# Optimization experiments

Measured on AMD Instinct MI355X. Metric: run time of the kernel, lower is better.

The kernel has to match this reference:

```python
import jax, jax.numpy as jnp
import numpy as np

D_MODEL = 1024
NUM_HEADS = 16
D_K = D_MODEL // NUM_HEADS


def setup_inputs() -> dict:
    key = jax.random.key(0)
    ks = jax.random.split(key, 9)
    B, S = 4, 2048
    s = 1.0 / np.sqrt(D_MODEL)
    inp = {
        "x": jax.random.normal(ks[0], (B, S, D_MODEL), dtype=jnp.float32),
        "wq": jax.random.uniform(ks[1], (D_MODEL, D_MODEL), jnp.float32, -s, s),
        "bq": jax.random.uniform(ks[2], (D_MODEL,), jnp.float32, -s, s),
        "wk": jax.random.uniform(ks[3], (D_MODEL, D_MODEL), jnp.float32, -s, s),
        "bk": jax.random.uniform(ks[4], (D_MODEL,), jnp.float32, -s, s),
        "wv": jax.random.uniform(ks[5], (D_MODEL, D_MODEL), jnp.float32, -s, s),
        "bv": jax.random.uniform(ks[6], (D_MODEL,), jnp.float32, -s, s),
        "wo": jax.random.uniform(ks[7], (D_MODEL, D_MODEL), jnp.float32, -s, s),
        "bo": jax.random.uniform(ks[8], (D_MODEL,), jnp.float32, -s, s),
    }
    return inp


def reference(x, wq, bq, wk, bk, wv, bv, wo, bo):
    B, S, _ = x.shape
    H, Dk = NUM_HEADS, D_K
    # QKV projections; weights stored as (in, out) so y = x @ w + b
    q = (x @ wq + bq).reshape(B, S, H, Dk).transpose(0, 2, 1, 3)  # (B,H,S,Dk)
    k = (x @ wk + bk).reshape(B, S, H, Dk).transpose(0, 2, 1, 3)
    v = (x @ wv + bv).reshape(B, S, H, Dk).transpose(0, 2, 1, 3)
    scores = jnp.einsum("bhqd,bhkd->bhqk", q, k) / jnp.sqrt(jnp.float32(Dk))
    causal = jnp.tril(jnp.ones((S, S), dtype=bool))  # True = keep
    scores = jnp.where(causal, scores, jnp.float32(-jnp.inf))
    attn = jax.nn.softmax(scores, axis=-1)  # dropout=0 (eval)
    out = jnp.einsum("bhqk,bhkd->bhqd", attn, v)
    out = out.transpose(0, 2, 1, 3).reshape(B, S, H * Dk)
    return out @ wo + bo
```

## Files before the change

kernel.cpp:

```cpp
#include <hip/hip_runtime.h>
#include <hip/hip_bf16.h>


#define D_MODEL 1024
#define NHEADS  16
#define DK      64
#define BATCH   4
#define SEQ     2048
#define MROWS   (BATCH*SEQ)

typedef short bvec8 __attribute__((ext_vector_type(8)));
typedef float fvec4  __attribute__((ext_vector_type(4)));
typedef float fvec16 __attribute__((ext_vector_type(16)));

__device__ __forceinline__ unsigned short f2bf(float f) {
    unsigned int x = __float_as_uint(f);
    x += 0x7fffu + ((x >> 16) & 1u);
    return (unsigned short)(x >> 16);
}
__device__ __forceinline__ float bf2f(unsigned short u) {
    return __uint_as_float(((unsigned int)u) << 16);
}

__device__ __forceinline__ unsigned pack_bf16x2(float a, float b) {
#if __has_builtin(__builtin_amdgcn_cvt_pk_bf16_f32)
    typedef __bf16 bf16x2_t __attribute__((ext_vector_type(2)));
    union { bf16x2_t v; unsigned u; } cv;
    cv.v = __builtin_amdgcn_cvt_pk_bf16_f32(a, b);
    return cv.u;
#else
    return (unsigned)f2bf(a) | ((unsigned)f2bf(b) << 16);
#endif
}

__device__ __forceinline__ float fast_exp2(float x) {
#if __has_builtin(__builtin_amdgcn_exp2f)
    return __builtin_amdgcn_exp2f(x);
#else
    return exp2f(x);
#endif
}


__global__ void f32_to_bf16_k(const float* __restrict__ in,
                              unsigned short* __restrict__ out, int n4) {
    int i = blockIdx.x * 256 + threadIdx.x;
    if (i < n4) {
        float4 v = ((const float4*)in)[i];
        ushort4 o;
        o.x = f2bf(v.x); o.y = f2bf(v.y); o.z = f2bf(v.z); o.w = f2bf(v.w);
        ((ushort4*)out)[i] = o;
    }
}

__global__ void transpose_all_k(const float* __restrict__ wq, const float* __restrict__ wk,
                                const float* __restrict__ wv, const float* __restrict__ wo,
                                unsigned short* __restrict__ wqkvt,
                                unsigned short* __restrict__ wot) {
    __shared__ float tile[32][33];
    const int z = blockIdx.z;
    const float* W = (z == 0) ? wq : (z == 1) ? wk : (z == 2) ? wv : wo;
    unsigned short* Wt = (z == 3) ? wot : wqkvt + (size_t)z * D_MODEL * D_MODEL;
    int n0 = blockIdx.x * 32, k0 = blockIdx.y * 32;
    int tx = threadIdx.x & 31;
    int ty = (threadIdx.x >> 5) * 4;
#pragma unroll
    for (int i = 0; i < 4; ++i)
        tile[ty + i][tx] = W[(k0 + ty + i) * D_MODEL + n0 + tx];
    __syncthreads();
#pragma unroll
    for (int i = 0; i < 4; ++i)
        Wt[(n0 + ty + i) * D_MODEL + k0 + tx] = f2bf(tile[tx][ty + i]);
}

__global__ void build_cbias_k(const float* __restrict__ bq, const float* __restrict__ bk,
                              const float* __restrict__ bv, float* __restrict__ cb) {
    int i = blockIdx.x * 256 + threadIdx.x;
    float v = (i < 1024) ? bq[i] : (i < 2048) ? bk[i - 1024] : bv[i - 2048];
    cb[i] = v;
}

__global__ __launch_bounds__(256, 2)
void gemm_glds(const unsigned short* __restrict__ A,
               const unsigned short* __restrict__ Bt,
               const float* __restrict__ bias,
               unsigned short* __restrict__ oq,
               unsigned short* __restrict__ ok,
               unsigned short* __restrict__ ov,
               float* __restrict__ of,
               float qscale, int mode) {
    __shared__ __align__(16) unsigned short As[2][128 * 64];
    __shared__ __align__(16) unsigned short Bs[2][128 * 64];

    const int tid  = threadIdx.x;
    const int lane = tid & 63;
    const int w    = tid >> 6;
    const int wr   = w >> 1, wc = w & 1;
    const int quad = lane >> 4, l16 = lane & 15;
    const int rowBlock = blockIdx.y * 128;
    const int colBlock = blockIdx.x * 128;

    const int lrow   = lane >> 3;
    const int gchunk = (lane & 7) ^ lrow;

    fvec4 acc[4][4] = {};

    {
#pragma unroll
        for (int n = 0; n < 4; ++n) {
            const int g = w * 4 + n;
            __builtin_amdgcn_global_load_lds(
                (const __attribute__((address_space(1))) void*)
                    &A[(size_t)(rowBlock + g * 8 + lrow) * D_MODEL + gchunk * 8],
                (__attribute__((address_space(3))) void*)&As[0][g * 512], 16, 0, 0);
            __builtin_amdgcn_global_load_lds(
                (const __attribute__((address_space(1))) void*)
                    &Bt[(size_t)(colBlock + g * 8 + lrow) * D_MODEL + gchunk * 8],
                (__attribute__((address_space(3))) void*)&Bs[0][g * 512], 16, 0, 0);
        }
    }

    for (int i = 0; i < 16; ++i) {
        __syncthreads();
        const int buf = i & 1;
        if (i < 15) {
            const int k1 = (i + 1) * 64;
#pragma unroll
            for (int n = 0; n < 4; ++n) {
                const int g = w * 4 + n;
                __builtin_amdgcn_global_load_lds(
                    (const __attribute__((address_space(1))) void*)
                        &A[(size_t)(rowBlock + g * 8 + lrow) * D_MODEL + k1 + gchunk * 8],
                    (__attribute__((address_space(3))) void*)&As[buf ^ 1][g * 512], 16, 0, 0);
                __builtin_amdgcn_global_load_lds(
                    (const __attribute__((address_space(1))) void*)
                        &Bt[(size_t)(colBlock + g * 8 + lrow) * D_MODEL + k1 + gchunk * 8],
                    (__attribute__((address_space(3))) void*)&Bs[buf ^ 1][g * 512], 16, 0, 0);
            }
        }
#pragma unroll
        for (int kc = 0; kc < 2; ++kc) {
            bvec8 af[4], bfr[4];
#pragma unroll
            for (int ii = 0; ii < 4; ++ii) {
                int r = wr * 64 + ii * 16 + l16;
                af[ii] = *(const bvec8*)&As[buf][r * 64 + (((kc * 4 + quad) ^ (l16 & 7)) * 8)];
            }
#pragma unroll
            for (int j = 0; j < 4; ++j) {
                int r = wc * 64 + j * 16 + l16;
                bfr[j] = *(const bvec8*)&Bs[buf][r * 64 + (((kc * 4 + quad) ^ (l16 & 7)) * 8)];
            }
#pragma unroll
            for (int ii = 0; ii < 4; ++ii)
#pragma unroll
                for (int j = 0; j < 4; ++j)
                    acc[ii][j] = __builtin_amdgcn_mfma_f32_16x16x32_bf16(
                        af[ii], bfr[j], acc[ii][j], 0, 0, 0);
        }
    }

    if (mode == 0) {
#pragma unroll
        for (int i = 0; i < 4; ++i) {
#pragma unroll
            for (int j = 0; j < 4; ++j) {
                int ncol = colBlock + wc * 64 + j * 16 + l16;
                int which = ncol >> 10;
                int nn = ncol & 1023;
                int h = nn >> 6, d = nn & 63;
                float bv = bias[ncol];
#pragma unroll
                for (int r = 0; r < 4; ++r) {
                    int mrow = rowBlock + wr * 64 + i * 16 + quad * 4 + r;
                    int b = mrow >> 11, s = mrow & (SEQ - 1);
                    float v = acc[i][j][r] + bv;
                    if (which == 0)
                        oq[(((b * NHEADS + h) * SEQ + s) * DK) + d] = f2bf(v * qscale);
                    else if (which == 1)
                        ok[(((b * NHEADS + h) * SEQ + s) * DK) + d] = f2bf(v);
                    else
                        ov[(((b * NHEADS + h) * DK + d) * SEQ) + s] = f2bf(v);
                }
            }
        }
    } else {
#pragma unroll
        for (int i = 0; i < 4; ++i) {
#pragma unroll
            for (int j = 0; j < 4; ++j) {
                int ncol = colBlock + wc * 64 + j * 16 + l16;
                float bv = bias[ncol];
#pragma unroll
                for (int r = 0; r < 4; ++r) {
                    int mrow = rowBlock + wr * 64 + i * 16 + quad * 4 + r;
                    of[(size_t)mrow * D_MODEL + ncol] = acc[i][j][r] + bv;
                }
            }
        }
    }
}

__global__ __launch_bounds__(256, 4)
void attn_mfmaA(const unsigned short* __restrict__ Q,
                const unsigned short* __restrict__ K,
                const unsigned short* __restrict__ Vt,
                unsigned short* __restrict__ O,
                unsigned short* __restrict__ Opart,
                float* __restrict__ Lpart) {
    __shared__ __align__(16) unsigned short Ksm[2][64 * 64];
    __shared__ __align__(16) unsigned short Vsm[2][64 * 64];
    __shared__ float Lsh[4][32];

    const int tid  = threadIdx.x;
    const int lane = tid & 63;
    const int wq   = tid >> 6;
    const int hf   = lane >> 5;
    const int l32  = lane & 31;
    const int hh = blockIdx.y, b = blockIdx.z;
    const int hb = b * NHEADS + hh;

    static const int qt_tbl[24] = {15,15,7,14,14,6,13,13,12,12,5,11,
                                   11,10,10,4,9,9,8,8,3,2,1,0};
    static const int md_tbl[24] = {0,1,2,0,1,2,0,1,0,1,2,0,
                                   1,0,1,2,0,1,0,1,2,2,2,2};
    const int bx = blockIdx.x;
    const int qt = qt_tbl[bx];
    const int md = md_tbl[bx];
    const bool part = (md < 2);
    const int kt0 = (md == 1) ? qt + 1 : 0;
    const int kt1 = (md == 0) ? qt + 1 : 2 * qt + 2;
    const int slot = part ? ((qt - 8) * 2 + md) : 0;

    const size_t bhq = ((size_t)hb) * SEQ * DK;
    const unsigned short* Qb = Q + bhq;
    const unsigned short* Kb = K + bhq;
    const unsigned short* Vb = Vt + bhq;

    const int q0 = qt * 128 + wq * 32;

    bvec8 qf[4];
#pragma unroll
    for (int kc = 0; kc < 4; ++kc)
        qf[kc] = *(const bvec8*)&Qb[(q0 + l32) * DK + kc * 16 + hf * 8];

    const int sr = tid >> 2;
    const int sc = tid & 3;
    const int sp0 = ((sc) ^ (sr & 7)) * 8;
    const int sp1 = ((sc + 4) ^ (sr & 7)) * 8;

    const int ktact = 2 * qt + (wq >> 1);
    const int mofs  = (wq & 1) << 5;

    bvec8 kr0, kr1, vr0, vr1;
    {
        const unsigned short* kg = Kb + (kt0 * 64 + sr) * DK;
        kr0 = *(const bvec8*)(kg + sc * 8);
        kr1 = *(const bvec8*)(kg + (sc + 4) * 8);
        const unsigned short* vg = Vb + sr * SEQ + kt0 * 64;
        vr0 = *(const bvec8*)(vg + sc * 8);
        vr1 = *(const bvec8*)(vg + (sc + 4) * 8);
        *(bvec8*)&Ksm[0][sr * 64 + sp0] = kr0;
        *(bvec8*)&Ksm[0][sr * 64 + sp1] = kr1;
        *(bvec8*)&Vsm[0][sr * 64 + sp0] = vr0;
        *(bvec8*)&Vsm[0][sr * 64 + sp1] = vr1;
    }

    fvec16 acc0 = {};
    fvec16 acc1 = {};
    float lp = 0.f;

    for (int kt = kt0; kt < kt1; ++kt) {
        __syncthreads();
        const int buf = (kt - kt0) & 1;
        if (kt + 1 < kt1) {
            const unsigned short* kg = Kb + ((kt + 1) * 64 + sr) * DK;
            kr0 = *(const bvec8*)(kg + sc * 8);
            kr1 = *(const bvec8*)(kg + (sc + 4) * 8);
            const unsigned short* vg = Vb + sr * SEQ + (kt + 1) * 64;
            vr0 = *(const bvec8*)(vg + sc * 8);
            vr1 = *(const bvec8*)(vg + (sc + 4) * 8);
        }
        if (kt <= ktact) {
            const unsigned short* Kbuf = &Ksm[buf][0];
            const unsigned short* Vbuf = &Vsm[buf][0];

            fvec16 s0 = {}, s1 = {};
            __builtin_amdgcn_s_setprio(1);
#pragma unroll
            for (int kc = 0; kc < 4; ++kc) {
                const int ch = (((kc * 2 + hf) ^ (l32 & 7)) * 8);
                bvec8 a0 = *(const bvec8*)&Kbuf[l32 * 64 + ch];
                bvec8 a1 = *(const bvec8*)&Kbuf[(32 + l32) * 64 + ch];
                s0 = __builtin_amdgcn_mfma_f32_32x32x16_bf16(a0, qf[kc], s0, 0, 0, 0);
                s1 = __builtin_amdgcn_mfma_f32_32x32x16_bf16(a1, qf[kc], s1, 0, 0, 0);
            }
            __builtin_amdgcn_s_setprio(0);

            if (kt == ktact) {
#pragma unroll
                for (int r = 0; r < 16; ++r) {
                    const int key0 = (r & 3) + 8 * (r >> 2) + 4 * hf - mofs;
                    if (key0 > l32)      s0[r] = -__builtin_inff();
                    if (key0 + 32 > l32) s1[r] = -__builtin_inff();
                }
            }

            unsigned pk[16];
#pragma unroll
            for (int m = 0; m < 8; ++m) {
                float p0 = fast_exp2(s0[2 * m]);
                float p1 = fast_exp2(s0[2 * m + 1]);
                float p2 = fast_exp2(s1[2 * m]);
                float p3 = fast_exp2(s1[2 * m + 1]);
                lp += (p0 + p1) + (p2 + p3);
                pk[m]     = pack_bf16x2(p0, p1);
                pk[8 + m] = pack_bf16x2(p2, p3);
            }

            __builtin_amdgcn_s_setprio(1);
#pragma unroll
            for (int kc16 = 0; kc16 < 4; ++kc16) {
                const int b0 = (kc16 >> 1) * 8 + (kc16 & 1) * 4;
                unsigned sw0 = __shfl_xor(pk[b0 + 0], 32);
                unsigned sw1 = __shfl_xor(pk[b0 + 1], 32);
                unsigned sw2 = __shfl_xor(pk[b0 + 2], 32);
                unsigned sw3 = __shfl_xor(pk[b0 + 3], 32);
                union { unsigned u[4]; bvec8 v; } afu;
                afu.u[0] = hf ? sw2 : pk[b0 + 0];
                afu.u[1] = hf ? sw3 : pk[b0 + 1];
                afu.u[2] = hf ? pk[b0 + 2] : sw0;
                afu.u[3] = hf ? pk[b0 + 3] : sw1;
                const int ch = (((kc16 * 2 + hf) ^ (l32 & 7)) * 8);
                bvec8 bv0 = *(const bvec8*)&Vbuf[l32 * 64 + ch];
                bvec8 bv1 = *(const bvec8*)&Vbuf[(32 + l32) * 64 + ch];
                acc0 = __builtin_amdgcn_mfma_f32_32x32x16_bf16(afu.v, bv0, acc0, 0, 0, 0);
                acc1 = __builtin_amdgcn_mfma_f32_32x32x16_bf16(afu.v, bv1, acc1, 0, 0, 0);
            }
            __builtin_amdgcn_s_setprio(0);
        }
        if (kt + 1 < kt1) {
            const int nb = ((kt - kt0) & 1) ^ 1;
            *(bvec8*)&Ksm[nb][sr * 64 + sp0] = kr0;
            *(bvec8*)&Ksm[nb][sr * 64 + sp1] = kr1;
            *(bvec8*)&Vsm[nb][sr * 64 + sp0] = vr0;
            *(bvec8*)&Vsm[nb][sr * 64 + sp1] = vr1;
        }
    }

    const float l = lp + __shfl_xor(lp, 32);

    if (part) {
        if (lane < 32)
            Lpart[((size_t)slot * 64 + hb) * 128 + wq * 32 + l32] = l;
        unsigned short* Od = Opart + (((size_t)slot * 64 + hb) * 128 + wq * 32) * 64;
#pragma unroll
        for (int g = 0; g < 4; ++g)
#pragma unroll
            for (int rr = 0; rr < 4; ++rr) {
                const int reg = g * 4 + rr;
                const int qrl = g * 8 + 4 * hf + rr;
                Od[(size_t)qrl * 64 + l32]      = f2bf(acc0[reg]);
                Od[(size_t)qrl * 64 + 32 + l32] = f2bf(acc1[reg]);
            }
    } else {
        if (lane < 32) Lsh[wq][l32] = l;
#pragma unroll
        for (int g = 0; g < 4; ++g) {
            float4 lv = *(const float4*)&Lsh[wq][g * 8 + 4 * hf];
#pragma unroll
            for (int rr = 0; rr < 4; ++rr) {
                const int reg = g * 4 + rr;
                const int qrow = q0 + g * 8 + 4 * hf + rr;
                const float inv = 1.f / ((const float*)&lv)[rr];
                unsigned short* dst = O + (size_t)(b * SEQ + qrow) * D_MODEL + hh * DK + l32;
                dst[0]  = f2bf(acc0[reg] * inv);
                dst[32] = f2bf(acc1[reg] * inv);
            }
        }
    }
}

__global__ void attn_combine_k(const unsigned short* __restrict__ Opart,
                               const float* __restrict__ Lpart,
                               unsigned short* __restrict__ O) {
    const int qt = 8 + blockIdx.x;
    const int h = blockIdx.y, b = blockIdx.z;
    const int hb = b * NHEADS + h;
    const int s0 = (qt - 8) * 2;
    const unsigned short* A  = Opart + ((size_t)(s0)*64 + hb) * 128 * 64;
    const unsigned short* Bp = Opart + ((size_t)(s0 + 1) * 64 + hb) * 128 * 64;
    const float* LA = Lpart + ((size_t)(s0)*64 + hb) * 128;
    const float* LB = Lpart + ((size_t)(s0 + 1) * 64 + hb) * 128;
    for (int e = threadIdx.x; e < 128 * 64; e += 256) {
        const int qr = e >> 6, d = e & 63;
        const float inv = 1.f / (LA[qr] + LB[qr]);
        const float v = (bf2f(A[e]) + bf2f(Bp[e])) * inv;
        O[(size_t)(b * SEQ + qt * 128 + qr) * D_MODEL + h * DK + d] = f2bf(v);
    }
}


extern "C" void kernel_launch(void* const* d_in, const int* in_sizes, int n_in,
                              void* d_out, int out_size, void* d_ws, size_t ws_size,
                              hipStream_t stream) {
    const float* x  = (const float*)d_in[0];
    const float* wq = (const float*)d_in[1];
    const float* bq = (const float*)d_in[2];
    const float* wk = (const float*)d_in[3];
    const float* bk = (const float*)d_in[4];
    const float* wv = (const float*)d_in[5];
    const float* bv = (const float*)d_in[6];
    const float* wo = (const float*)d_in[7];
    const float* bo = (const float*)d_in[8];
    float* out = (float*)d_out;

    char* ws = (char*)d_ws;
    const size_t MB = 1u << 20;
    unsigned short* xb    = (unsigned short*)(ws);
    unsigned short* wqkvt = (unsigned short*)(ws + 16 * MB);
    unsigned short* wot   = (unsigned short*)(ws + 22 * MB);
    unsigned short* qb    = (unsigned short*)(ws + 24 * MB);
    unsigned short* kb    = (unsigned short*)(ws + 40 * MB);
    unsigned short* vtb   = (unsigned short*)(ws + 56 * MB);
    unsigned short* ab    = (unsigned short*)(ws + 72 * MB);
    float* cbias = (float*)(ws + 72 * MB);
    unsigned short* Opart = (unsigned short*)(ws);
    float* Lpart = (float*)(ws + 16 * MB);

    f32_to_bf16_k<<<(MROWS * D_MODEL / 4 + 255) / 256, 256, 0, stream>>>(
        x, xb, MROWS * D_MODEL / 4);
    transpose_all_k<<<dim3(32, 32, 4), 256, 0, stream>>>(wq, wk, wv, wo, wqkvt, wot);
    build_cbias_k<<<12, 256, 0, stream>>>(bq, bk, bv, cbias);

    const float QSCALE = 0.125f * 1.44269504088896340736f;

    gemm_glds<<<dim3(3072 / 128, MROWS / 128), 256, 0, stream>>>(
        xb, wqkvt, cbias, qb, kb, vtb, nullptr, QSCALE, 0);

    attn_mfmaA<<<dim3(24, NHEADS, BATCH), 256, 0, stream>>>(
        qb, kb, vtb, ab, Opart, Lpart);
    attn_combine_k<<<dim3(8, NHEADS, BATCH), 256, 0, stream>>>(Opart, Lpart, ab);

    gemm_glds<<<dim3(D_MODEL / 128, MROWS / 128), 256, 0, stream>>>(
        ab, wot, bo, nullptr, nullptr, nullptr, out, 1.0f, 1);
}
```

Baseline: 295.1 us.

## Add 256x256-tile QKV GEMM with 4-stage direct-to-LDS pipeline

Measured after the change: 320.6 us. 8.6% more time.

```diff
diff --git a/kernel.cpp b/kernel.cpp
--- a/kernel.cpp
+++ b/kernel.cpp
@@ -80,15 +80,123 @@
     cb[i] = v;
 }
 
+__global__ __launch_bounds__(512, 2)
+void gemm_qkv_q8(const unsigned short* __restrict__ A,
+                 const unsigned short* __restrict__ Bt,
+                 const float* __restrict__ bias,
+                 unsigned short* __restrict__ oq,
+                 unsigned short* __restrict__ ok,
+                 unsigned short* __restrict__ ov,
+                 float qscale) {
+    __shared__ __align__(16) unsigned short Abuf[4][256 * 32];
+    __shared__ __align__(16) unsigned short Bbuf[4][256 * 32];
+
+    const int tid  = threadIdx.x;
+    const int lane = tid & 63;
+    const int w    = tid >> 6;
+    const int wm   = w >> 2;
+    const int wn   = w & 3;
+    const int quad = lane >> 4, l16 = lane & 15;
+    const int rowBlock = blockIdx.y * 256;
+    const int colBlock = blockIdx.x * 256;
+
+    const int srow = tid >> 2;
+    const int skc  = (tid & 3) ^ ((srow >> 1) & 3);
+    const size_t aoff0 = (size_t)(rowBlock + srow) * D_MODEL + skc * 8;
+    const size_t boff0 = (size_t)(colBlock + srow) * D_MODEL + skc * 8;
+    const size_t roff1 = (size_t)128 * D_MODEL;
+
+#define Q8_STAGE(u) do {                                                      \
+    const int _b = (u) & 3; const int _k = (u) * 32;                          \
+    __builtin_amdgcn_global_load_lds(                                         \
+        (const __attribute__((address_space(1))) void*)(A + aoff0 + _k),      \
+        (__attribute__((address_space(3))) void*)&Abuf[_b][tid * 8], 16, 0, 0); \
+    __builtin_amdgcn_global_load_lds(                                         \
+        (const __attribute__((address_space(1))) void*)(A + aoff0 + roff1 + _k), \
+        (__attribute__((address_space(3))) void*)&Abuf[_b][(tid + 512) * 8], 16, 0, 0); \
+    __builtin_amdgcn_global_load_lds(                                         \
+        (const __attribute__((address_space(1))) void*)(Bt + boff0 + _k),     \
+        (__attribute__((address_space(3))) void*)&Bbuf[_b][tid * 8], 16, 0, 0); \
+    __builtin_amdgcn_global_load_lds(                                         \
+        (const __attribute__((address_space(1))) void*)(Bt + boff0 + roff1 + _k), \
+        (__attribute__((address_space(3))) void*)&Bbuf[_b][(tid + 512) * 8], 16, 0, 0); \
+} while (0)
+
+    fvec4 acc[8][4] = {};
+    const int sw = quad ^ ((l16 >> 1) & 3);
+
+    Q8_STAGE(0); Q8_STAGE(1); Q8_STAGE(2);
+
+#define Q8_COMPUTE(PH) do {                                                   \
+    const unsigned short* Au = &Abuf[(PH) & 3][0];                            \
+    const unsigned short* Bu = &Bbuf[(PH) & 3][0];                            \
+    bvec8 af[8], bfr[4];                                                      \
+    _Pragma("unroll")                                                         \
+    for (int mf = 0; mf < 8; ++mf) {                                          \
+        const int row = wm * 128 + mf * 16 + l16;                             \
+        af[mf] = *(const bvec8*)&Au[(row * 4 + sw) * 8];                      \
+    }                                                                         \
+    _Pragma("unroll")                                                         \
+    for (int nf = 0; nf < 4; ++nf) {                                          \
+        const int nrow = wn * 64 + nf * 16 + l16;                             \
+        bfr[nf] = *(const bvec8*)&Bu[(nrow * 4 + sw) * 8];                    \
+    }                                                                         \
+    __builtin_amdgcn_s_setprio(1);                                            \
+    _Pragma("unroll")                                                         \
+    for (int mf = 0; mf < 8; ++mf)                                            \
+        _Pragma("unroll")                                                     \
+        for (int nf = 0; nf < 4; ++nf)                                        \
+            acc[mf][nf] = __builtin_amdgcn_mfma_f32_16x16x32_bf16(            \
+                af[mf], bfr[nf], acc[mf][nf], 0, 0, 0);                       \
+    __builtin_amdgcn_s_setprio(0);                                            \
+} while (0)
+
+    for (int ph = 0; ph < 30; ++ph) {
+        asm volatile("s_waitcnt vmcnt(8)" ::: "memory");
+        __builtin_amdgcn_s_barrier();
+        if (ph < 29) Q8_STAGE(ph + 3);
+        Q8_COMPUTE(ph);
+    }
+    asm volatile("s_waitcnt vmcnt(4)" ::: "memory");
+    __builtin_amdgcn_s_barrier();
+    Q8_COMPUTE(30);
+    asm volatile("s_waitcnt vmcnt(0)" ::: "memory");
+    __builtin_amdgcn_s_barrier();
+    Q8_COMPUTE(31);
+
+#undef Q8_STAGE
+#undef Q8_COMPUTE
+
+#pragma unroll
+    for (int mf = 0; mf < 8; ++mf) {
+#pragma unroll
+        for (int nf = 0; nf < 4; ++nf) {
+            const int ncol = colBlock + wn * 64 + nf * 16 + l16;
+            const int which = ncol >> 10;
+            const int nn = ncol & 1023;
+            const int h = nn >> 6, d = nn & 63;
+            const float bv = bias[ncol];
+#pragma unroll
+            for (int r = 0; r < 4; ++r) {
+                const int mrow = rowBlock + wm * 128 + mf * 16 + quad * 4 + r;
+                const int b = mrow >> 11, s = mrow & (SEQ - 1);
+                const float v = acc[mf][nf][r] + bv;
+                if (which == 0)
+                    oq[(((b * NHEADS + h) * SEQ + s) * DK) + d] = f2bf(v * qscale);
+                else if (which == 1)
+                    ok[(((b * NHEADS + h) * SEQ + s) * DK) + d] = f2bf(v);
+                else
+                    ov[(((b * NHEADS + h) * DK + d) * SEQ) + s] = f2bf(v);
+            }
+        }
+    }
+}
+
 __global__ __launch_bounds__(256, 2)
 void gemm_glds(const unsigned short* __restrict__ A,
                const unsigned short* __restrict__ Bt,
                const float* __restrict__ bias,
-               unsigned short* __restrict__ oq,
-               unsigned short* __restrict__ ok,
-               unsigned short* __restrict__ ov,
-               float* __restrict__ of,
-               float qscale, int mode) {
+               float* __restrict__ of) {
     __shared__ __align__(16) unsigned short As[2][128 * 64];
     __shared__ __align__(16) unsigned short Bs[2][128 * 64];
 
@@ -160,42 +268,16 @@
         }
     }
 
-    if (mode == 0) {
-#pragma unroll
-        for (int i = 0; i < 4; ++i) {
-#pragma unroll
-            for (int j = 0; j < 4; ++j) {
-                int ncol = colBlock + wc * 64 + j * 16 + l16;
-                int which = ncol >> 10;
-                int nn = ncol & 1023;
-                int h = nn >> 6, d = nn & 63;
-                float bv = bias[ncol];
-#pragma unroll
-                for (int r = 0; r < 4; ++r) {
-                    int mrow = rowBlock + wr * 64 + i * 16 + quad * 4 + r;
-                    int b = mrow >> 11, s = mrow & (SEQ - 1);
-                    float v = acc[i][j][r] + bv;
-                    if (which == 0)
-                        oq[(((b * NHEADS + h) * SEQ + s) * DK) + d] = f2bf(v * qscale);
-                    else if (which == 1)
-                        ok[(((b * NHEADS + h) * SEQ + s) * DK) + d] = f2bf(v);
-                    else
-                        ov[(((b * NHEADS + h) * DK + d) * SEQ) + s] = f2bf(v);
-                }
-            }
-        }
-    } else {
-#pragma unroll
-        for (int i = 0; i < 4; ++i) {
-#pragma unroll
-            for (int j = 0; j < 4; ++j) {
-                int ncol = colBlock + wc * 64 + j * 16 + l16;
-                float bv = bias[ncol];
-#pragma unroll
-                for (int r = 0; r < 4; ++r) {
-                    int mrow = rowBlock + wr * 64 + i * 16 + quad * 4 + r;
-                    of[(size_t)mrow * D_MODEL + ncol] = acc[i][j][r] + bv;
-                }
+#pragma unroll
+    for (int i = 0; i < 4; ++i) {
+#pragma unroll
+        for (int j = 0; j < 4; ++j) {
+            int ncol = colBlock + wc * 64 + j * 16 + l16;
+            float bv = bias[ncol];
+#pragma unroll
+            for (int r = 0; r < 4; ++r) {
+                int mrow = rowBlock + wr * 64 + i * 16 + quad * 4 + r;
+                of[(size_t)mrow * D_MODEL + ncol] = acc[i][j][r] + bv;
             }
         }
     }
@@ -435,13 +517,13 @@
 
     const float QSCALE = 0.125f * 1.44269504088896340736f;
 
-    gemm_glds<<<dim3(3072 / 128, MROWS / 128), 256, 0, stream>>>(
-        xb, wqkvt, cbias, qb, kb, vtb, nullptr, QSCALE, 0);
+    gemm_qkv_q8<<<dim3(3072 / 256, MROWS / 256), 512, 0, stream>>>(
+        xb, wqkvt, cbias, qb, kb, vtb, QSCALE);
 
     attn_mfmaA<<<dim3(24, NHEADS, BATCH), 256, 0, stream>>>(
         qb, kb, vtb, ab, Opart, Lpart);
     attn_combine_k<<<dim3(8, NHEADS, BATCH), 256, 0, stream>>>(Opart, Lpart, ab);
 
     gemm_glds<<<dim3(D_MODEL / 128, MROWS / 128), 256, 0, stream>>>(
-        ab, wot, bo, nullptr, nullptr, nullptr, out, 1.0f, 1);
-}
+        ab, wot, bo, out);
+}
```
